# Kernel tuning notes

Measured on AMD Instinct MI355X. Metric: run time of the kernel, lower is better.

## Reference

```python
import jax, jax.numpy as jnp
import numpy as np
from jax import lax

TOP_K = 2
NHEAD = 8

def _ln(x, g, b, eps=1e-5):
    m = x.mean(-1, keepdims=True)
    v = x.var(-1, keepdims=True)
    return (x - m) / jnp.sqrt(v + eps) * g + b


def setup_inputs() -> dict:
    B, S, N = 32, 512, 32
    DT, D, E, HE, MO, LTX, LTCN, K = 64, 128, 16, 256, 128, 2, 4, 3
    keys = iter(jax.random.split(jax.random.key(0), 96))
    def rn(shape, s=0.05):
        return (jax.random.normal(next(keys), shape, jnp.float32) * s)
    inp = {}
    inp['x_features_globally_std'] = jax.random.normal(next(keys), (B, S, N), jnp.float32)
    counts = jax.random.randint(next(keys), (B,), 8, N + 1)
    inp['sensor_mask'] = (jnp.arange(N)[None, :] < counts[:, None]).astype(jnp.float32)
    inp['proj_w'] = rn((1, DT)); inp['proj_b'] = jnp.zeros(DT)
    inp['tcn_w1'] = rn((LTCN, DT, DT, K)); inp['tcn_b1'] = jnp.zeros((LTCN, DT))
    inp['tcn_w2'] = rn((LTCN, DT, DT, K)); inp['tcn_b2'] = jnp.zeros((LTCN, DT))
    inp['tcn_ln_g'] = jnp.ones(DT); inp['tcn_ln_b'] = jnp.zeros(DT)
    inp['pool_w'] = rn((DT, D)); inp['pool_b'] = jnp.zeros(D)
    inp['pos_inter'] = rn((1, N, D), 0.02)
    inp['tx_ln1_g'] = jnp.ones((LTX, D)); inp['tx_ln1_b'] = jnp.zeros((LTX, D))
    inp['tx_qkv_w'] = rn((LTX, D, 3 * D)); inp['tx_qkv_b'] = jnp.zeros((LTX, 3 * D))
    inp['tx_out_w'] = rn((LTX, D, D)); inp['tx_out_b'] = jnp.zeros((LTX, D))
    inp['tx_ln2_g'] = jnp.ones((LTX, D)); inp['tx_ln2_b'] = jnp.zeros((LTX, D))
    inp['tx_ff1_w'] = rn((LTX, D, 2 * D)); inp['tx_ff1_b'] = jnp.zeros((LTX, 2 * D))
    inp['tx_ff2_w'] = rn((LTX, 2 * D, D)); inp['tx_ff2_b'] = jnp.zeros((LTX, D))
    inp['tx_fln_g'] = jnp.ones(D); inp['tx_fln_b'] = jnp.zeros(D)
    inp['exp_w1'] = rn((E, D, HE)); inp['exp_b1'] = jnp.zeros((E, HE))
    inp['exp_w2'] = rn((E, HE, MO)); inp['exp_b2'] = jnp.zeros((E, MO))
    inp['gate_f_w'] = rn((2 * D, E)); inp['gate_f_b'] = jnp.zeros(E)
    inp['gate_fail_w'] = rn((2 * D, E)); inp['gate_fail_b'] = jnp.zeros(E)
    inp['gate_rca_w'] = rn((D, E)); inp['gate_rca_b'] = jnp.zeros(E)
    inp['pred_w'] = rn((DT + D + MO, 3)); inp['pred_b'] = jnp.zeros(3)
    inp['fail_w'] = rn((MO, 3)); inp['fail_b'] = jnp.zeros(3)
    inp['rca_w'] = rn((DT + D + MO, 1)); inp['rca_b'] = jnp.zeros(1)
    return inp


def reference(x_features_globally_std, sensor_mask, proj_w, proj_b, tcn_w1, tcn_b1, tcn_w2, tcn_b2,
              tcn_ln_g, tcn_ln_b, pool_w, pool_b, pos_inter, tx_ln1_g, tx_ln1_b, tx_qkv_w, tx_qkv_b,
              tx_out_w, tx_out_b, tx_ln2_g, tx_ln2_b, tx_ff1_w, tx_ff1_b, tx_ff2_w, tx_ff2_b,
              tx_fln_g, tx_fln_b, exp_w1, exp_b1, exp_w2, exp_b2, gate_f_w, gate_f_b,
              gate_fail_w, gate_fail_b, gate_rca_w, gate_rca_b, pred_w, pred_b, fail_w, fail_b, rca_w, rca_b):
    x = x_features_globally_std
    B, S, N = x.shape
    DT = proj_w.shape[1]; D = pool_w.shape[1]; E = gate_f_b.shape[0]
    K = tcn_w1.shape[-1]
    # per-sensor encoder: [B,S,N] -> [B*N, S, 1]
    x_enc = x.transpose(0, 2, 1).reshape(B * N, S, 1)
    h = x_enc @ proj_w + proj_b  # [BN,S,DT]
    # sinusoidal positional encoding
    pos = jnp.arange(S, dtype=jnp.float32)[:, None]
    div = jnp.exp(jnp.arange(0, DT, 2, dtype=jnp.float32) * (-np.log(10000.0) / DT))
    pe = jnp.zeros((S, DT), jnp.float32).at[:, 0::2].set(jnp.sin(pos * div)).at[:, 1::2].set(jnp.cos(pos * div))
    h = h + pe
    h = h.transpose(0, 2, 1)  # [BN, DT, S]
    for i in range(tcn_w1.shape[0]):
        dil = 2 ** i
        pad = (K - 1) * dil  # causal left pad == torch pad-both + trim right
        def conv(z, w, b):
            return lax.conv_general_dilated(z, w, (1,), [(pad, 0)], rhs_dilation=(dil,),
                                            dimension_numbers=('NCH', 'OIH', 'NCH')) + b[None, :, None]
        o = jax.nn.relu(conv(h, tcn_w1[i], tcn_b1[i]))
        o = jax.nn.relu(conv(o, tcn_w2[i], tcn_b2[i]))
        h = jax.nn.relu(o + h)  # proj_dim == tcn_out_dim -> no downsample
    h = _ln(h.transpose(0, 2, 1), tcn_ln_g, tcn_ln_b)  # [BN,S,DT]
    st = h.reshape(B, N, S, DT) * sensor_mask[:, :, None, None]
    pooled = st.mean(2)  # [B,N,DT]
    z = pooled @ pool_w + pool_b  # [B,N,D]
    z = z + pos_inter[0, :N]
    pad_mask = sensor_mask == 0  # [B,N] True = padded key
    hd = D // NHEAD
    for l in range(tx_qkv_w.shape[0]):
        y = _ln(z, tx_ln1_g[l], tx_ln1_b[l])
        qkv = y @ tx_qkv_w[l] + tx_qkv_b[l]
        q, k_, v = jnp.split(qkv, 3, -1)
        q = q.reshape(B, N, NHEAD, hd).transpose(0, 2, 1, 3)
        k_ = k_.reshape(B, N, NHEAD, hd).transpose(0, 2, 1, 3)
        v = v.reshape(B, N, NHEAD, hd).transpose(0, 2, 1, 3)
        scores = jnp.einsum('bhqd,bhkd->bhqk', q, k_) / jnp.sqrt(jnp.float32(hd))
        scores = jnp.where(pad_mask[:, None, None, :], -1e9, scores)
        attn = jax.nn.softmax(scores, -1)
        o = jnp.einsum('bhqk,bhkd->bhqd', attn, v).transpose(0, 2, 1, 3).reshape(B, N, D)
        z = z + o @ tx_out_w[l] + tx_out_b[l]
        y = _ln(z, tx_ln2_g[l], tx_ln2_b[l])
        z = z + jax.nn.relu(y @ tx_ff1_w[l] + tx_ff1_b[l]) @ tx_ff2_w[l] + tx_ff2_b[l]
    z = _ln(z, tx_fln_g, tx_fln_b)
    ctx = z * sensor_mask[..., None]  # [B,N,D]
    cnt = jnp.clip(sensor_mask.sum(1, keepdims=True), 1.0, None)
    mean_ctx = ctx.sum(1) / cnt
    var_ctx = (ctx ** 2).sum(1) / cnt - mean_ctx ** 2
    router_in = jnp.concatenate([mean_ctx, jnp.sqrt(jnp.clip(var_ctx, 1e-6, None))], -1)  # [B,2D]

    def moe(xin, gin, gw, gb):
        logits = gin @ gw + gb  # [n,E]
        tv, ti = lax.top_k(logits, TOP_K)
        w = jax.nn.softmax(tv, -1)
        h1 = jax.nn.relu(jnp.einsum('nd,edh->neh', xin, exp_w1) + exp_b1)
        allo = jnp.einsum('neh,eho->neo', h1, exp_w2) + exp_b2  # dense all-expert, per torch code
        sel = jnp.take_along_axis(allo, ti[:, :, None], 1)
        y = (sel * w[:, :, None]).sum(1)
        probs = jax.nn.softmax(logits, -1)
        frac = jnp.zeros((E,), probs.dtype).at[ti.reshape(-1)].add(1.0) / (xin.shape[0] * TOP_K)
        loss = E * (probs.mean(0) * frac).sum()
        return y, loss

    moe_f, aux_f = moe(mean_ctx, router_in, gate_f_w, gate_f_b)
    moe_fail, _ = moe(mean_ctx, router_in, gate_fail_w, gate_fail_b)
    tok = ctx.reshape(B * N, D)
    moe_rca, _ = moe(tok, tok, gate_rca_w, gate_rca_b)
    moe_rca = (moe_rca * sensor_mask.reshape(-1, 1)).reshape(B, N, -1)  # zero invalid tokens
    st_last = st[:, :, -1, :]  # [B,N,DT]
    moe_f_exp = jnp.broadcast_to(moe_f[:, None, :], (B, N, moe_f.shape[-1]))
    pred_in = jnp.concatenate([st_last, ctx, moe_f_exp], -1)
    pred = pred_in @ pred_w + pred_b  # [B,N,pred_horizons]
    fail = moe_fail @ fail_w + fail_b  # [B,fail_horizons]
    rca_in = jnp.concatenate([st_last, ctx, moe_rca], -1)
    rca = (rca_in @ rca_w + rca_b)[..., 0]  # [B,N]
    return pred, fail, rca, aux_f
```

## Files before the change

### kernel.cpp

```cpp
#include <hip/hip_runtime.h>
#include <hip/hip_bf16.h>
#include <math.h>

typedef short short8v __attribute__((ext_vector_type(8)));
typedef float f32x4 __attribute__((ext_vector_type(4)));
typedef unsigned short ushort4v __attribute__((ext_vector_type(4)));

__device__ inline float waveReduceSum(float v){
  #pragma unroll
  for (int off = 32; off > 0; off >>= 1) v += __shfl_xor(v, off, 64);
  return v;
}

__device__ inline unsigned short f2bf(float x){
  unsigned int u = __builtin_bit_cast(unsigned int, x);
  unsigned int r = (u + 0x7FFFu + ((u >> 16) & 1u)) >> 16;
  return (unsigned short)r;
}
__device__ inline float bf2f(unsigned short u){
  unsigned int w = ((unsigned int)u) << 16;
  return __builtin_bit_cast(float, w);
}

__global__ void init_kernel(const float* __restrict__ w1, const float* __restrict__ w2,
                            unsigned short* __restrict__ wf, float* __restrict__ petab){
  int idx = blockIdx.x * 256 + threadIdx.x;
  if (idx < 98304){
    int conv = idx / 12288;
    int r = idx % 12288;
    int tap = r >> 12;
    int kk  = (r >> 11) & 1;
    int ct  = (r >> 9) & 3;
    int lane= (r >> 3) & 63;
    int j   = r & 7;
    int layer = conv >> 1;
    const float* src = (conv & 1) ? w2 : w1;
    int co = (ct << 4) + (lane & 15);
    int ci = (kk << 5) + ((lane >> 4) << 3) + j;
    float v = src[((layer * 64 + co) * 64 + ci) * 3 + tap];
    unsigned short hi = f2bf(v);
    unsigned short lo = f2bf(v - bf2f(hi));
    size_t base = (size_t)conv * 24576 + (size_t)(((tap * 2 + kk) * 4 + ct) * 2) * 512 + lane * 8 + j;
    wf[base] = hi;
    wf[base + 512] = lo;
  } else if (idx < 131072){
    int p = idx - 98304;
    int t = p >> 6, c = p & 63;
    float ang = (float)t * expf(-0.14391156831f * (float)(c & ~1));
    petab[p] = (c & 1) ? cosf(ang) : sinf(ang);
  }
}

__global__ __launch_bounds__(512, 2) void tcn_persist_kernel(
    const float* __restrict__ x, const unsigned short* __restrict__ wfrag,
    const float* __restrict__ b1g, const float* __restrict__ b2g,
    const float* __restrict__ petab,
    const float* __restrict__ pw, const float* __restrict__ pb,
    const float* __restrict__ lng, const float* __restrict__ lnb,
    const float* __restrict__ maskg,
    float* __restrict__ pooled, float* __restrict__ stlast){
  constexpr int O_OFF = 139264;
  constexpr int P_OFF = 159744;
  __shared__ __align__(16) char lds[161792];
  const int tid = threadIdx.x;
  const int lane = tid & 63, wid = tid >> 6;
  const int cp = wid & 1, tsub = wid >> 1;
  const int bn = blockIdx.x;
  const int bb = bn >> 5, nn = bn & 31;

  for (int i = 0; i < 9; ++i){
    int idx = tid + i * 512;
    if (idx < 4352){
      int row = idx >> 3, cg = idx & 7;
      int t = row - 32;
      short8v vh = {0,0,0,0,0,0,0,0}, vl = {0,0,0,0,0,0,0,0};
      if (t >= 0){
        float xv = x[((size_t)bb << 14) + (t << 5) + nn];
        const float* per = petab + t * 64 + cg * 8;
        #pragma unroll
        for (int j = 0; j < 8; ++j){
          int c = cg * 8 + j;
          float val = fmaf(xv, pw[c], pb[c]) + per[j];
          unsigned short h = f2bf(val);
          vh[j] = (short)h;
          vl[j] = (short)f2bf(val - bf2f(h));
        }
      }
      int sw = (row & 7) << 4;
      int base = (row << 8) + (cg << 4);
      *(short8v*)(lds + (base ^ sw)) = vh;
      *(short8v*)(lds + ((base + 128) ^ sw)) = vl;
    }
  }

  const int cobase0 = ((2 * cp) << 4) + ((lane >> 4) << 2);
  const int cobase1 = ((2 * cp + 1) << 4) + ((lane >> 4) << 2);

  for (int layer = 0; layer < 4; ++layer){
    const int dil = 1 << layer;
    const int convbase = layer * 2;
    f32x4 b1v0 = *(const f32x4*)(b1g + (layer << 6) + cobase0);
    f32x4 b1v1 = *(const f32x4*)(b1g + (layer << 6) + cobase1);
    f32x4 b2v0 = *(const f32x4*)(b2g + (layer << 6) + cobase0);
    f32x4 b2v1 = *(const f32x4*)(b2g + (layer << 6) + cobase1);

    for (int ch = 7; ch >= 0; --ch){
      const int t0 = ch << 6;
      __syncthreads();

      short8v A1[3][2][2][2];
      #pragma unroll
      for (int tap = 0; tap < 3; ++tap)
        #pragma unroll
        for (int kk = 0; kk < 2; ++kk)
          #pragma unroll
          for (int cc = 0; cc < 2; ++cc)
            #pragma unroll
            for (int pl = 0; pl < 2; ++pl){
              int ct = 2 * cp + cc;
              A1[tap][kk][cc][pl] = *(const short8v*)(wfrag + (size_t)convbase * 24576 +
                  (size_t)((((tap * 2 + kk) * 4 + ct) * 2 + pl)) * 512 + lane * 8);
            }

      for (int S = 0; S < 2; ++S){
        int rbase = (S << 6) + (tsub << 4);
        if (rbase >= 80) continue;
        f32x4 acc0 = {0.f,0.f,0.f,0.f}, acc1 = {0.f,0.f,0.f,0.f};
        int orow = rbase + (lane & 15);
        int t_o = t0 - 16 + orow;
        #pragma unroll
        for (int tap = 0; tap < 3; ++tap){
          int hr = t_o - (2 - tap) * dil + 32;
          int sw = (hr & 7) << 4;
          #pragma unroll
          for (int kk = 0; kk < 2; ++kk){
            int base = (hr << 8) + (kk << 6) + ((lane >> 4) << 4);
            short8v Bhi = *(const short8v*)(lds + (base ^ sw));
            short8v Blo = *(const short8v*)(lds + ((base + 128) ^ sw));
            acc0 = __builtin_amdgcn_mfma_f32_16x16x32_bf16(A1[tap][kk][0][0], Bhi, acc0, 0, 0, 0);
            acc0 = __builtin_amdgcn_mfma_f32_16x16x32_bf16(A1[tap][kk][0][0], Blo, acc0, 0, 0, 0);
            acc0 = __builtin_amdgcn_mfma_f32_16x16x32_bf16(A1[tap][kk][0][1], Bhi, acc0, 0, 0, 0);
            acc1 = __builtin_amdgcn_mfma_f32_16x16x32_bf16(A1[tap][kk][1][0], Bhi, acc1, 0, 0, 0);
            acc1 = __builtin_amdgcn_mfma_f32_16x16x32_bf16(A1[tap][kk][1][0], Blo, acc1, 0, 0, 0);
            acc1 = __builtin_amdgcn_mfma_f32_16x16x32_bf16(A1[tap][kk][1][1], Bhi, acc1, 0, 0, 0);
          }
        }
        int swO = (orow & 7) << 4;
        #pragma unroll
        for (int cc = 0; cc < 2; ++cc){
          int cobase = (cc == 0) ? cobase0 : cobase1;
          ushort4v hi4, lo4;
          #pragma unroll
          for (int r = 0; r < 4; ++r){
            float a = (cc == 0) ? acc0[r] : acc1[r];
            float bv = (cc == 0) ? b1v0[r] : b1v1[r];
            float v = fmaxf(a + bv, 0.f);
            if (t_o < 0) v = 0.f;
            unsigned short h = f2bf(v);
            hi4[r] = h;
            lo4[r] = f2bf(v - bf2f(h));
          }
          int ob = O_OFF + (orow << 8) + (cobase << 1);
          *(ushort4v*)(lds + (ob ^ swO)) = hi4;
          *(ushort4v*)(lds + ((ob + 128) ^ swO)) = lo4;
        }
      }

      short8v A2[3][2][2][2];
      #pragma unroll
      for (int tap = 0; tap < 3; ++tap)
        #pragma unroll
        for (int kk = 0; kk < 2; ++kk)
          #pragma unroll
          for (int cc = 0; cc < 2; ++cc)
            #pragma unroll
            for (int pl = 0; pl < 2; ++pl){
              int ct = 2 * cp + cc;
              A2[tap][kk][cc][pl] = *(const short8v*)(wfrag + (size_t)(convbase + 1) * 24576 +
                  (size_t)((((tap * 2 + kk) * 4 + ct) * 2 + pl)) * 512 + lane * 8);
            }
      __syncthreads();

      {
        f32x4 acc0 = {0.f,0.f,0.f,0.f}, acc1 = {0.f,0.f,0.f,0.f};
        int tt = (tsub << 4) + (lane & 15);
        #pragma unroll
        for (int tap = 0; tap < 3; ++tap){
          int ol = tt + 16 - (2 - tap) * dil;
          int sw = (ol & 7) << 4;
          #pragma unroll
          for (int kk = 0; kk < 2; ++kk){
            int base = O_OFF + (ol << 8) + (kk << 6) + ((lane >> 4) << 4);
            short8v Bhi = *(const short8v*)(lds + (base ^ sw));
            short8v Blo = *(const short8v*)(lds + ((base + 128) ^ sw));
            acc0 = __builtin_amdgcn_mfma_f32_16x16x32_bf16(A2[tap][kk][0][0], Bhi, acc0, 0, 0, 0);
            acc0 = __builtin_amdgcn_mfma_f32_16x16x32_bf16(A2[tap][kk][0][0], Blo, acc0, 0, 0, 0);
            acc0 = __builtin_amdgcn_mfma_f32_16x16x32_bf16(A2[tap][kk][0][1], Bhi, acc0, 0, 0, 0);
            acc1 = __builtin_amdgcn_mfma_f32_16x16x32_bf16(A2[tap][kk][1][0], Bhi, acc1, 0, 0, 0);
            acc1 = __builtin_amdgcn_mfma_f32_16x16x32_bf16(A2[tap][kk][1][0], Blo, acc1, 0, 0, 0);
            acc1 = __builtin_amdgcn_mfma_f32_16x16x32_bf16(A2[tap][kk][1][1], Bhi, acc1, 0, 0, 0);
          }
        }
        int hr = t0 + tt + 32;
        int swH = (hr & 7) << 4;
        #pragma unroll
        for (int cc = 0; cc < 2; ++cc){
          int cobase = (cc == 0) ? cobase0 : cobase1;
          int rb = (hr << 8) + (cobase << 1);
          ushort4v rhi = *(const ushort4v*)(lds + (rb ^ swH));
          ushort4v rlo = *(const ushort4v*)(lds + ((rb + 128) ^ swH));
          ushort4v hi4, lo4;
          #pragma unroll
          for (int r = 0; r < 4; ++r){
            float a = (cc == 0) ? acc0[r] : acc1[r];
            float bv = (cc == 0) ? b2v0[r] : b2v1[r];
            float v = fmaxf(a + bv, 0.f);
            v = fmaxf(v + bf2f(rhi[r]) + bf2f(rlo[r]), 0.f);
            unsigned short h = f2bf(v);
            hi4[r] = h;
            lo4[r] = f2bf(v - bf2f(h));
          }
          *(ushort4v*)(lds + (rb ^ swH)) = hi4;
          *(ushort4v*)(lds + ((rb + 128) ^ swH)) = lo4;
        }
      }
    }
  }

  __syncthreads();
  {
    int s8 = tid >> 6, c = tid & 63;
    float gc = lng[c], bc = lnb[c];
    float mk = maskg[bn];
    float acc = 0.f, last = 0.f;
    for (int r0 = 0; r0 < 64; ++r0){
      int row = (s8 << 6) + r0;
      int hr = row + 32;
      int sw = (hr & 7) << 4;
      int base = (hr << 8) + (c << 1);
      float hi = bf2f(*(const unsigned short*)(lds + (base ^ sw)));
      float lo = bf2f(*(const unsigned short*)(lds + ((base + 128) ^ sw)));
      float val = hi + lo;
      float sum = val, sq = val * val;
      #pragma unroll
      for (int off = 32; off > 0; off >>= 1){
        sum += __shfl_xor(sum, off, 64);
        sq  += __shfl_xor(sq, off, 64);
      }
      float mean = sum * (1.f / 64.f);
      float var = sq * (1.f / 64.f) - mean * mean;
      float rstd = rsqrtf(var + 1e-5f);
      float o = (val - mean) * rstd * gc + bc;
      acc += o;
      if (row == 511) last = o;
    }
    *(float*)(lds + P_OFF + ((s8 << 6) + c) * 4) = acc;
    if (s8 == 7) stlast[(size_t)bn * 64 + c] = last * mk;
    __syncthreads();
    if (tid < 64){
      float tot = 0.f;
      #pragma unroll
      for (int ss = 0; ss < 8; ++ss) tot += *(const float*)(lds + P_OFF + ((ss << 6) + tid) * 4);
      pooled[(size_t)bn * 64 + tid] = tot * (1.f / 512.f) * mk;
    }
  }
}

__global__ __launch_bounds__(1024) void batch_kernel(
    const float* __restrict__ pooled, const float* __restrict__ maskg,
    const float* __restrict__ pool_w, const float* __restrict__ pool_b,
    const float* __restrict__ pos,
    const float* __restrict__ ln1g, const float* __restrict__ ln1b,
    const float* __restrict__ qkvw, const float* __restrict__ qkvb_g,
    const float* __restrict__ outw, const float* __restrict__ outb,
    const float* __restrict__ ln2g, const float* __restrict__ ln2b,
    const float* __restrict__ ff1w, const float* __restrict__ ff1b,
    const float* __restrict__ ff2w, const float* __restrict__ ff2b,
    const float* __restrict__ flng, const float* __restrict__ flnb,
    const float* __restrict__ ew1, const float* __restrict__ eb1,
    const float* __restrict__ ew2, const float* __restrict__ eb2,
    const float* __restrict__ gfw, const float* __restrict__ gfb,
    const float* __restrict__ gfailw, const float* __restrict__ gfailb,
    const float* __restrict__ failw, const float* __restrict__ failb,
    float* __restrict__ ctxg, float* __restrict__ moefg,
    float* __restrict__ logitsfg, int* __restrict__ tifg,
    float* __restrict__ outg){
  __shared__ float zf[32][128];
  __shared__ float ybuf[32][128];
  __shared__ float qkvb[32][385];
  __shared__ float sc[8][33][33];
  __shared__ float ps[32][64];
  __shared__ float msk[32];
  __shared__ float rin[256];
  __shared__ float meanc[128];
  __shared__ float h1all[4][256];
  __shared__ float oall[4][128];
  __shared__ float lf[16], lfail[16];
  __shared__ int   tisel[4];
  __shared__ float twsel[4];
  __shared__ float moefail[128];
  __shared__ float cntS;

  const int b = blockIdx.x;
  const int tid = threadIdx.x;
  const int lane = tid & 63;

  if (tid < 32) msk[tid] = maskg[b * 32 + tid];
  #pragma unroll
  for (int i = 0; i < 2; ++i){
    int item = tid + 1024 * i;
    int n = item >> 6, c = item & 63;
    ps[n][c] = pooled[(size_t)(b * 32 + n) * 64 + c];
  }
  __syncthreads();

  {
    int jb = tid & 63, nb = tid >> 6;
    float acc[2][2];
    #pragma unroll
    for (int nn = 0; nn < 2; ++nn)
      #pragma unroll
      for (int jj = 0; jj < 2; ++jj){
        int d = jb * 2 + jj, n = nb * 2 + nn;
        acc[nn][jj] = pool_b[d] + pos[n * 128 + d];
      }
    #pragma unroll 8
    for (int k = 0; k < 64; ++k){
      float w0 = pool_w[k * 128 + jb * 2], w1 = pool_w[k * 128 + jb * 2 + 1];
      #pragma unroll
      for (int nn = 0; nn < 2; ++nn){
        float y = ps[nb * 2 + nn][k];
        acc[nn][0] += y * w0; acc[nn][1] += y * w1;
      }
    }
    #pragma unroll
    for (int nn = 0; nn < 2; ++nn){
      zf[nb * 2 + nn][jb * 2]     = acc[nn][0];
      zf[nb * 2 + nn][jb * 2 + 1] = acc[nn][1];
    }
  }
  __syncthreads();

  for (int l = 0; l < 2; ++l){
    const float* Wq = qkvw + (size_t)l * 49152;
    const float* bq = qkvb_g + l * 384;
    const float* Wo = outw + (size_t)l * 16384;
    const float* bo = outb + l * 128;
    const float* W1 = ff1w + (size_t)l * 32768;
    const float* bf1 = ff1b + l * 256;
    const float* W2 = ff2w + (size_t)l * 32768;
    const float* bf2 = ff2b + l * 128;
    const float* g1 = ln1g + l * 128; const float* bb1 = ln1b + l * 128;
    const float* g2 = ln2g + l * 128; const float* bb2 = ln2b + l * 128;

    #pragma unroll
    for (int rr = 0; rr < 2; ++rr){
      int row = (tid >> 6) * 2 + rr;
      float x0 = zf[row][lane], x1 = zf[row][lane + 64];
      float mean = waveReduceSum(x0 + x1) * (1.f / 128.f);
      float d0 = x0 - mean, d1 = x1 - mean;
      float var = waveReduceSum(d0 * d0 + d1 * d1) * (1.f / 128.f);
      float rstd = rsqrtf(var + 1e-5f);
      ybuf[row][lane]      = d0 * rstd * g1[lane] + bb1[lane];
      ybuf[row][lane + 64] = d1 * rstd * g1[lane + 64] + bb1[lane + 64];
    }
    __syncthreads();

    {
      int jb = tid & 127, nb = tid >> 7;
      float acc[4][3];
      #pragma unroll
      for (int nn = 0; nn < 4; ++nn)
        #pragma unroll
        for (int jj = 0; jj < 3; ++jj) acc[nn][jj] = 0.f;
      #pragma unroll 8
      for (int k = 0; k < 128; ++k){
        float w0 = Wq[k * 384 + jb * 3], w1 = Wq[k * 384 + jb * 3 + 1], w2v = Wq[k * 384 + jb * 3 + 2];
        #pragma unroll
        for (int nn = 0; nn < 4; ++nn){
          float y = ybuf[nb * 4 + nn][k];
          acc[nn][0] += y * w0; acc[nn][1] += y * w1; acc[nn][2] += y * w2v;
        }
      }
      #pragma unroll
      for (int nn = 0; nn < 4; ++nn)
        #pragma unroll
        for (int jj = 0; jj < 3; ++jj)
          qkvb[nb * 4 + nn][jb * 3 + jj] = acc[nn][jj] + bq[jb * 3 + jj];
    }
    __syncthreads();

    #pragma unroll
    for (int i = 0; i < 8; ++i){
      int item = tid + 1024 * i;
      int hh = item >> 10, qi = (item >> 5) & 31, ki = item & 31;
      float a = 0.f;
      #pragma unroll
      for (int d = 0; d < 16; ++d) a += qkvb[qi][hh * 16 + d] * qkvb[ki][128 + hh * 16 + d];
      a *= 0.25f;
      if (msk[ki] == 0.f) a = -1e9f;
      sc[hh][qi][ki] = a;
    }
    __syncthreads();
    {
      int row = tid >> 2, q4 = tid & 3;
      int hh = row >> 5, qi = row & 31;
      float v[8];
      float m = -1e30f;
      #pragma unroll
      for (int j = 0; j < 8; ++j){ v[j] = sc[hh][qi][q4 * 8 + j]; m = fmaxf(m, v[j]); }
      m = fmaxf(m, __shfl_xor(m, 1, 64));
      m = fmaxf(m, __shfl_xor(m, 2, 64));
      float s = 0.f;
      #pragma unroll
      for (int j = 0; j < 8; ++j){ v[j] = expf(v[j] - m); s += v[j]; }
      s += __shfl_xor(s, 1, 64);
      s += __shfl_xor(s, 2, 64);
      float inv = 1.f / s;
      #pragma unroll
      for (int j = 0; j < 8; ++j) sc[hh][qi][q4 * 8 + j] = v[j] * inv;
    }
    __syncthreads();
    #pragma unroll
    for (int i = 0; i < 4; ++i){
      int item = tid + 1024 * i;
      int n = item >> 7, dd = item & 127, hh = dd >> 4;
      float o = 0.f;
      #pragma unroll
      for (int ki = 0; ki < 32; ++ki) o += sc[hh][n][ki] * qkvb[ki][256 + dd];
      ybuf[n][dd] = o;
    }
    __syncthreads();

    {
      int jb = tid & 63, nb = tid >> 6;
      float acc[2][2];
      #pragma unroll
      for (int nn = 0; nn < 2; ++nn){ acc[nn][0] = 0.f; acc[nn][1] = 0.f; }
      #pragma unroll 8
      for (int k = 0; k < 128; ++k){
        float w0 = Wo[k * 128 + jb * 2], w1 = Wo[k * 128 + jb * 2 + 1];
        #pragma unroll
        for (int nn = 0; nn < 2; ++nn){
          float y = ybuf[nb * 2 + nn][k];
          acc[nn][0] += y * w0; acc[nn][1] += y * w1;
        }
      }
      #pragma unroll
      for (int nn = 0; nn < 2; ++nn){
        zf[nb * 2 + nn][jb * 2]     += acc[nn][0] + bo[jb * 2];
        zf[nb * 2 + nn][jb * 2 + 1] += acc[nn][1] + bo[jb * 2 + 1];
      }
    }
    __syncthreads();

    #pragma unroll
    for (int rr = 0; rr < 2; ++rr){
      int row = (tid >> 6) * 2 + rr;
      float x0 = zf[row][lane], x1 = zf[row][lane + 64];
      float mean = waveReduceSum(x0 + x1) * (1.f / 128.f);
      float d0 = x0 - mean, d1 = x1 - mean;
      float var = waveReduceSum(d0 * d0 + d1 * d1) * (1.f / 128.f);
      float rstd = rsqrtf(var + 1e-5f);
      ybuf[row][lane]      = d0 * rstd * g2[lane] + bb2[lane];
      ybuf[row][lane + 64] = d1 * rstd * g2[lane + 64] + bb2[lane + 64];
    }
    __syncthreads();

    {
      int jb = tid & 127, nb = tid >> 7;
      float acc[4][2];
      #pragma unroll
      for (int nn = 0; nn < 4; ++nn){ acc[nn][0] = 0.f; acc[nn][1] = 0.f; }
      #pragma unroll 8
      for (int k = 0; k < 128; ++k){
        float w0 = W1[k * 256 + jb * 2], w1 = W1[k * 256 + jb * 2 + 1];
        #pragma unroll
        for (int nn = 0; nn < 4; ++nn){
          float y = ybuf[nb * 4 + nn][k];
          acc[nn][0] += y * w0; acc[nn][1] += y * w1;
        }
      }
      #pragma unroll
      for (int nn = 0; nn < 4; ++nn){
        qkvb[nb * 4 + nn][jb * 2]     = fmaxf(acc[nn][0] + bf1[jb * 2], 0.f);
        qkvb[nb * 4 + nn][jb * 2 + 1] = fmaxf(acc[nn][1] + bf1[jb * 2 + 1], 0.f);
      }
    }
    __syncthreads();

    {
      int jb = tid & 63, nb = tid >> 6;
      float acc[2][2];
      #pragma unroll
      for (int nn = 0; nn < 2; ++nn){ acc[nn][0] = 0.f; acc[nn][1] = 0.f; }
      #pragma unroll 8
      for (int k = 0; k < 256; ++k){
        float w0 = W2[k * 128 + jb * 2], w1 = W2[k * 128 + jb * 2 + 1];
        #pragma unroll
        for (int nn = 0; nn < 2; ++nn){
          float y = qkvb[nb * 2 + nn][k];
          acc[nn][0] += y * w0; acc[nn][1] += y * w1;
        }
      }
      #pragma unroll
      for (int nn = 0; nn < 2; ++nn){
        zf[nb * 2 + nn][jb * 2]     += acc[nn][0] + bf2[jb * 2];
        zf[nb * 2 + nn][jb * 2 + 1] += acc[nn][1] + bf2[jb * 2 + 1];
      }
    }
    __syncthreads();
  }

  #pragma unroll
  for (int rr = 0; rr < 2; ++rr){
    int row = (tid >> 6) * 2 + rr;
    float x0 = zf[row][lane], x1 = zf[row][lane + 64];
    float mean = waveReduceSum(x0 + x1) * (1.f / 128.f);
    float d0 = x0 - mean, d1 = x1 - mean;
    float var = waveReduceSum(d0 * d0 + d1 * d1) * (1.f / 128.f);
    float rstd = rsqrtf(var + 1e-5f);
    float mk = msk[row];
    ybuf[row][lane]      = (d0 * rstd * flng[lane] + flnb[lane]) * mk;
    ybuf[row][lane + 64] = (d1 * rstd * flng[lane + 64] + flnb[lane + 64]) * mk;
  }
  if (tid == 0){
    float c = 0.f;
    for (int n = 0; n < 32; ++n) c += maskg[b * 32 + n];
    cntS = fmaxf(c, 1.f);
  }
  __syncthreads();
  #pragma unroll
  for (int i = 0; i < 4; ++i){
    int item = tid + 1024 * i;
    int n = item >> 7, d = item & 127;
    ctxg[(size_t)(b * 32 + n) * 128 + d] = ybuf[n][d];
  }
  if (tid < 128){
    float s = 0.f, s2 = 0.f;
    #pragma unroll 8
    for (int n = 0; n < 32; ++n){ float v = ybuf[n][tid]; s += v; s2 += v * v; }
    float mean = s / cntS;
    float var = s2 / cntS - mean * mean;
    meanc[tid] = mean;
    rin[tid] = mean;
    rin[128 + tid] = sqrtf(fmaxf(var, 1e-6f));
  }
  __syncthreads();
  {
    int g = tid >> 9;
    int e = (tid >> 5) & 15, kk = tid & 31;
    const float* gw = g ? gfailw : gfw;
    float a = 0.f;
    #pragma unroll
    for (int j = 0; j < 8; ++j){
      int k = kk * 8 + j;
      a += rin[k] * gw[k * 16 + e];
    }
    a += __shfl_xor(a, 1, 64);  a += __shfl_xor(a, 2, 64);
    a += __shfl_xor(a, 4, 64);  a += __shfl_xor(a, 8, 64);
    a += __shfl_xor(a, 16, 64);
    if (kk == 0){
      if (g == 0){
        float r = a + gfb[e];
        lf[e] = r;
        logitsfg[b * 16 + e] = r;
      } else {
        lfail[e] = a + gfailb[e];
      }
    }
  }
  __syncthreads();
  if (tid < 2){
    const float* lg = (tid == 0) ? lf : lfail;
    int i0 = 0; float v0 = lg[0];
    for (int e = 1; e < 16; ++e) if (lg[e] > v0){ v0 = lg[e]; i0 = e; }
    int i1 = -1; float v1 = -1e30f;
    for (int e = 0; e < 16; ++e) if (e != i0 && lg[e] > v1){ v1 = lg[e]; i1 = e; }
    float e1 = expf(v1 - v0);
    float den = 1.f / (1.f + e1);
    tisel[tid * 2] = i0; tisel[tid * 2 + 1] = i1;
    twsel[tid * 2] = den; twsel[tid * 2 + 1] = e1 * den;
    if (tid == 0){ tifg[b * 2] = i0; tifg[b * 2 + 1] = i1; }
  }
  __syncthreads();
  {
    int sel = tid >> 8, h = tid & 255;
    int e = tisel[sel];
    float a = eb1[e * 256 + h];
    #pragma unroll 8
    for (int k = 0; k < 128; ++k) a += meanc[k] * ew1[(size_t)(e * 128 + k) * 256 + h];
    h1all[sel][h] = fmaxf(a, 0.f);
  }
  __syncthreads();
  if (tid < 512){
    int sel = tid >> 7, d = tid & 127;
    int e = tisel[sel];
    float o = eb2[e * 128 + d];
    #pragma unroll 8
    for (int k = 0; k < 256; ++k) o += h1all[sel][k] * ew2[(size_t)(e * 256 + k) * 128 + d];
    oall[sel][d] = twsel[sel] * o;
  }
  __syncthreads();
  if (tid < 128){
    moefg[b * 128 + tid] = oall[0][tid] + oall[1][tid];
    moefail[tid] = oall[2][tid] + oall[3][tid];
  }
  __syncthreads();
  if (tid < 3){
    float a = failb[tid];
    for (int k = 0; k < 128; ++k) a += moefail[k] * failw[k * 3 + tid];
    outg[3072 + b * 3 + tid] = a;
  }
}

__global__ void gate_kernel(const float* __restrict__ gin, const float* __restrict__ gw,
                            const float* __restrict__ gb, int ntok, int K,
                            int* __restrict__ ti, float* __restrict__ tw,
                            float* __restrict__ logits_out){
  int tok = blockIdx.x * 64 + threadIdx.x;
  if (tok >= ntok) return;
  float acc[16];
  #pragma unroll
  for (int e = 0; e < 16; ++e) acc[e] = gb[e];
  const float* gr = gin + (size_t)tok * K;
  #pragma unroll 4
  for (int k = 0; k < K; ++k){
    float gv = gr[k];
    #pragma unroll
    for (int e = 0; e < 16; ++e) acc[e] = fmaf(gv, gw[k*16 + e], acc[e]);
  }
  if (logits_out){
    #pragma unroll
    for (int e = 0; e < 16; ++e) logits_out[tok*16 + e] = acc[e];
  }
  int i0 = 0; float v0 = acc[0];
  #pragma unroll
  for (int e = 1; e < 16; ++e) if (acc[e] > v0){ v0 = acc[e]; i0 = e; }
  int i1 = -1; float v1 = -1e30f;
  #pragma unroll
  for (int e = 0; e < 16; ++e) if (e != i0 && acc[e] > v1){ v1 = acc[e]; i1 = e; }
  float e1 = expf(v1 - v0);
  float den = 1.f / (1.f + e1);
  ti[tok*2] = i0; ti[tok*2+1] = i1;
  tw[tok*2] = den; tw[tok*2+1] = e1 * den;
}

__global__ void moe_expert_kernel(const float* __restrict__ xin, const int* __restrict__ ti,
                                  const float* __restrict__ tw,
                                  const float* __restrict__ w1, const float* __restrict__ b1,
                                  const float* __restrict__ w2, const float* __restrict__ b2,
                                  const float* __restrict__ mask, float* __restrict__ yout){
  int tok = blockIdx.x;
  int tid = threadIdx.x;
  __shared__ float xs[128];
  __shared__ float h1[256];
  if (tid < 128) xs[tid] = xin[(size_t)tok*128 + tid];
  __syncthreads();
  float accv = 0.f;
  for (int kkk = 0; kkk < 2; ++kkk){
    int e = ti[tok*2 + kkk];
    float wv = tw[tok*2 + kkk];
    float a = b1[e*256 + tid];
    #pragma unroll 8
    for (int k = 0; k < 128; ++k) a = fmaf(xs[k], w1[(size_t)(e*128 + k)*256 + tid], a);
    __syncthreads();
    h1[tid] = fmaxf(a, 0.f);
    __syncthreads();
    if (tid < 128){
      float o = b2[e*128 + tid];
      #pragma unroll 8
      for (int k = 0; k < 256; ++k) o = fmaf(h1[k], w2[(size_t)(e*256 + k)*128 + tid], o);
      accv += wv * o;
    }
  }
  if (tid < 128){
    if (mask) accv *= mask[tok];
    yout[(size_t)tok*128 + tid] = accv;
  }
}

__global__ void aux_kernel(const float* __restrict__ logits, const int* __restrict__ ti,
                           float* __restrict__ out_scalar){
  if (threadIdx.x != 0 || blockIdx.x != 0) return;
  float pm[16];
  for (int e = 0; e < 16; ++e) pm[e] = 0.f;
  for (int i = 0; i < 32; ++i){
    const float* row = logits + i*16;
    float m = -1e30f;
    for (int e = 0; e < 16; ++e) m = fmaxf(m, row[e]);
    float s = 0.f;
    float ex[16];
    for (int e = 0; e < 16; ++e){ ex[e] = expf(row[e] - m); s += ex[e]; }
    for (int e = 0; e < 16; ++e) pm[e] += ex[e] / s;
  }
  float cnt[16];
  for (int e = 0; e < 16; ++e) cnt[e] = 0.f;
  for (int i = 0; i < 64; ++i) cnt[ti[i]] += 1.f;
  float loss = 0.f;
  for (int e = 0; e < 16; ++e) loss += (pm[e] / 32.f) * (cnt[e] / 64.f);
  out_scalar[0] = 16.f * loss;
}

__global__ void heads_kernel(const float* __restrict__ st_last, const float* __restrict__ ctx,
                             const float* __restrict__ moe_f, const float* __restrict__ moe_rca,
                             const float* __restrict__ pred_w, const float* __restrict__ pred_b,
                             const float* __restrict__ rca_w, const float* __restrict__ rca_b,
                             float* __restrict__ out){
  int bn = blockIdx.x * 256 + threadIdx.x;
  if (bn >= 1024) return;
  int b = bn >> 5;
  float p0 = pred_b[0], p1 = pred_b[1], p2 = pred_b[2];
  float r = rca_b[0];
  #pragma unroll 4
  for (int i = 0; i < 64; ++i){
    float v = st_last[(size_t)bn*64 + i];
    p0 = fmaf(v, pred_w[i*3+0], p0); p1 = fmaf(v, pred_w[i*3+1], p1); p2 = fmaf(v, pred_w[i*3+2], p2);
    r = fmaf(v, rca_w[i], r);
  }
  #pragma unroll 4
  for (int i = 0; i < 128; ++i){
    float v = ctx[(size_t)bn*128 + i];
    int ii = 64 + i;
    p0 = fmaf(v, pred_w[ii*3+0], p0); p1 = fmaf(v, pred_w[ii*3+1], p1); p2 = fmaf(v, pred_w[ii*3+2], p2);
    r = fmaf(v, rca_w[ii], r);
  }
  #pragma unroll 4
  for (int i = 0; i < 128; ++i){
    int ii = 192 + i;
    float vp = moe_f[(size_t)b*128 + i];
    p0 = fmaf(vp, pred_w[ii*3+0], p0); p1 = fmaf(vp, pred_w[ii*3+1], p1); p2 = fmaf(vp, pred_w[ii*3+2], p2);
    float vr = moe_rca[(size_t)bn*128 + i];
    r = fmaf(vr, rca_w[ii], r);
  }
  out[bn*3+0] = p0; out[bn*3+1] = p1; out[bn*3+2] = p2;
  out[3168 + bn] = r;
}

extern "C" void kernel_launch(void* const* d_in, const int* in_sizes, int n_in,
                              void* d_out, int out_size, void* d_ws, size_t ws_size,
                              hipStream_t stream){
  const float* x        = (const float*)d_in[0];
  const float* mask     = (const float*)d_in[1];
  const float* proj_w   = (const float*)d_in[2];
  const float* proj_b   = (const float*)d_in[3];
  const float* tcn_w1   = (const float*)d_in[4];
  const float* tcn_b1   = (const float*)d_in[5];
  const float* tcn_w2   = (const float*)d_in[6];
  const float* tcn_b2   = (const float*)d_in[7];
  const float* tcn_ln_g = (const float*)d_in[8];
  const float* tcn_ln_b = (const float*)d_in[9];
  const float* pool_w   = (const float*)d_in[10];
  const float* pool_b   = (const float*)d_in[11];
  const float* pos_inter= (const float*)d_in[12];
  const float* tx_ln1_g = (const float*)d_in[13];
  const float* tx_ln1_b = (const float*)d_in[14];
  const float* tx_qkv_w = (const float*)d_in[15];
  const float* tx_qkv_b = (const float*)d_in[16];
  const float* tx_out_w = (const float*)d_in[17];
  const float* tx_out_b = (const float*)d_in[18];
  const float* tx_ln2_g = (const float*)d_in[19];
  const float* tx_ln2_b = (const float*)d_in[20];
  const float* tx_ff1_w = (const float*)d_in[21];
  const float* tx_ff1_b = (const float*)d_in[22];
  const float* tx_ff2_w = (const float*)d_in[23];
  const float* tx_ff2_b = (const float*)d_in[24];
  const float* tx_fln_g = (const float*)d_in[25];
  const float* tx_fln_b = (const float*)d_in[26];
  const float* exp_w1   = (const float*)d_in[27];
  const float* exp_b1   = (const float*)d_in[28];
  const float* exp_w2   = (const float*)d_in[29];
  const float* exp_b2   = (const float*)d_in[30];
  const float* gate_f_w = (const float*)d_in[31];
  const float* gate_f_b = (const float*)d_in[32];
  const float* gate_fail_w = (const float*)d_in[33];
  const float* gate_fail_b = (const float*)d_in[34];
  const float* gate_rca_w  = (const float*)d_in[35];
  const float* gate_rca_b  = (const float*)d_in[36];
  const float* pred_w   = (const float*)d_in[37];
  const float* pred_b   = (const float*)d_in[38];
  const float* fail_w   = (const float*)d_in[39];
  const float* fail_b   = (const float*)d_in[40];
  const float* rca_w    = (const float*)d_in[41];
  const float* rca_b    = (const float*)d_in[42];
  float* out = (float*)d_out;
  float* W = (float*)d_ws;

  const size_t o_pooled  = 0;
  const size_t o_stlast  = 65536;
  const size_t o_ctx     = 131072;
  const size_t o_moef    = 262144;
  const size_t o_moerca  = 266240;
  const size_t o_logitsf = 397312;
  const size_t o_tif     = 397824;
  const size_t o_twrca   = 397888;
  const size_t o_tirca   = 399936;
  const size_t o_petab   = 401984;
  unsigned short* wfragU = (unsigned short*)(W + 434752);

  init_kernel<<<512, 256, 0, stream>>>(tcn_w1, tcn_w2, wfragU, W + o_petab);

  tcn_persist_kernel<<<1024, 512, 0, stream>>>(
      x, wfragU, tcn_b1, tcn_b2, W + o_petab, proj_w, proj_b,
      tcn_ln_g, tcn_ln_b, mask, W + o_pooled, W + o_stlast);

  batch_kernel<<<32, 1024, 0, stream>>>(
      W + o_pooled, mask, pool_w, pool_b, pos_inter,
      tx_ln1_g, tx_ln1_b, tx_qkv_w, tx_qkv_b, tx_out_w, tx_out_b,
      tx_ln2_g, tx_ln2_b, tx_ff1_w, tx_ff1_b, tx_ff2_w, tx_ff2_b,
      tx_fln_g, tx_fln_b,
      exp_w1, exp_b1, exp_w2, exp_b2,
      gate_f_w, gate_f_b, gate_fail_w, gate_fail_b, fail_w, fail_b,
      W + o_ctx, W + o_moef, W + o_logitsf, (int*)(W + o_tif), out);

  gate_kernel<<<16, 64, 0, stream>>>(W + o_ctx, gate_rca_w, gate_rca_b, 1024, 128,
                                     (int*)(W + o_tirca), W + o_twrca, nullptr);
  moe_expert_kernel<<<1024, 256, 0, stream>>>(W + o_ctx, (int*)(W + o_tirca), W + o_twrca,
                                              exp_w1, exp_b1, exp_w2, exp_b2, mask, W + o_moerca);

  aux_kernel<<<1, 64, 0, stream>>>(W + o_logitsf, (int*)(W + o_tif), out + 4192);
  heads_kernel<<<4, 256, 0, stream>>>(W + o_stlast, W + o_ctx, W + o_moef, W + o_moerca,
                                      pred_w, pred_b, rca_w, rca_b, out);
}
```

Baseline: 944.1 us.

## Double TCN block to 1024 threads with one output tile per wave

The TCN kernel now launches 1024 threads per block, so each wave handles one 16-channel output tile instead of two. This halves per-wave weight fragments and accumulators, and layers become templated for compile-time dilation. The pooled-reduction scratch reuses the intermediate buffer region, which adds a barrier, and the LayerNorm pass is split across 16 waves. Each wave has less MFMA work to hide latency, and register pressure under the 1024-thread launch bound may cause spills.

```diff
diff --git a/kernel.cpp b/kernel.cpp
--- a/kernel.cpp
+++ b/kernel.cpp
@@ -21,6 +21,8 @@
   unsigned int w = ((unsigned int)u) << 16;
   return __builtin_bit_cast(float, w);
 }
+
+#define TCN_O_OFF 139264
 
 __global__ void init_kernel(const float* __restrict__ w1, const float* __restrict__ w2,
                             unsigned short* __restrict__ wf, float* __restrict__ petab){
@@ -51,7 +53,117 @@
   }
 }
 
-__global__ __launch_bounds__(512, 2) void tcn_persist_kernel(
+template<int LAYER>
+__device__ __forceinline__ void run_layer(
+    char* lds, const unsigned short* __restrict__ wfrag,
+    const float* __restrict__ b1g, const float* __restrict__ b2g,
+    int lane, int coq, int tsub){
+  constexpr int DIL = 1 << LAYER;
+  constexpr int CONVBASE = LAYER * 2;
+  const int cobase = (coq << 4) + ((lane >> 4) << 2);
+  const f32x4 b1v = *(const f32x4*)(b1g + (LAYER << 6) + cobase);
+  const f32x4 b2v = *(const f32x4*)(b2g + (LAYER << 6) + cobase);
+
+  for (int ch = 7; ch >= 0; --ch){
+    const int t0 = ch << 6;
+    __syncthreads();
+
+    short8v A1[3][2][2];
+    #pragma unroll
+    for (int tap = 0; tap < 3; ++tap)
+      #pragma unroll
+      for (int kk = 0; kk < 2; ++kk)
+        #pragma unroll
+        for (int pl = 0; pl < 2; ++pl)
+          A1[tap][kk][pl] = *(const short8v*)(wfrag + (size_t)CONVBASE * 24576 +
+              (size_t)((((tap * 2 + kk) * 4 + coq) * 2 + pl)) * 512 + lane * 8);
+
+    #pragma unroll
+    for (int S = 0; S < 2; ++S){
+      int rbase = (S << 6) + (tsub << 4);
+      if (rbase < 80){
+        f32x4 acc = {0.f,0.f,0.f,0.f};
+        int orow = rbase + (lane & 15);
+        int t_o = t0 - 16 + orow;
+        #pragma unroll
+        for (int tap = 0; tap < 3; ++tap){
+          int hr = t_o - (2 - tap) * DIL + 32;
+          int sw = (hr & 7) << 4;
+          #pragma unroll
+          for (int kk = 0; kk < 2; ++kk){
+            int base = (hr << 8) + (kk << 6) + ((lane >> 4) << 4);
+            short8v Bhi = *(const short8v*)(lds + (base ^ sw));
+            short8v Blo = *(const short8v*)(lds + ((base + 128) ^ sw));
+            acc = __builtin_amdgcn_mfma_f32_16x16x32_bf16(A1[tap][kk][0], Bhi, acc, 0, 0, 0);
+            acc = __builtin_amdgcn_mfma_f32_16x16x32_bf16(A1[tap][kk][0], Blo, acc, 0, 0, 0);
+            acc = __builtin_amdgcn_mfma_f32_16x16x32_bf16(A1[tap][kk][1], Bhi, acc, 0, 0, 0);
+          }
+        }
+        int swO = (orow & 7) << 4;
+        ushort4v hi4, lo4;
+        #pragma unroll
+        for (int r = 0; r < 4; ++r){
+          float v = fmaxf(acc[r] + b1v[r], 0.f);
+          if (t_o < 0) v = 0.f;
+          unsigned short h = f2bf(v);
+          hi4[r] = h;
+          lo4[r] = f2bf(v - bf2f(h));
+        }
+        int ob = TCN_O_OFF + (orow << 8) + (cobase << 1);
+        *(ushort4v*)(lds + (ob ^ swO)) = hi4;
+        *(ushort4v*)(lds + ((ob + 128) ^ swO)) = lo4;
+      }
+    }
+
+    short8v A2[3][2][2];
+    #pragma unroll
+    for (int tap = 0; tap < 3; ++tap)
+      #pragma unroll
+      for (int kk = 0; kk < 2; ++kk)
+        #pragma unroll
+        for (int pl = 0; pl < 2; ++pl)
+          A2[tap][kk][pl] = *(const short8v*)(wfrag + (size_t)(CONVBASE + 1) * 24576 +
+              (size_t)((((tap * 2 + kk) * 4 + coq) * 2 + pl)) * 512 + lane * 8);
+    __syncthreads();
+
+    {
+      f32x4 acc = {0.f,0.f,0.f,0.f};
+      int tt = (tsub << 4) + (lane & 15);
+      #pragma unroll
+      for (int tap = 0; tap < 3; ++tap){
+        int ol = tt + 16 - (2 - tap) * DIL;
+        int sw = (ol & 7) << 4;
+        #pragma unroll
+        for (int kk = 0; kk < 2; ++kk){
+          int base = TCN_O_OFF + (ol << 8) + (kk << 6) + ((lane >> 4) << 4);
+          short8v Bhi = *(const short8v*)(lds + (base ^ sw));
+          short8v Blo = *(const short8v*)(lds + ((base + 128) ^ sw));
+          acc = __builtin_amdgcn_mfma_f32_16x16x32_bf16(A2[tap][kk][0], Bhi, acc, 0, 0, 0);
+          acc = __builtin_amdgcn_mfma_f32_16x16x32_bf16(A2[tap][kk][0], Blo, acc, 0, 0, 0);
+          acc = __builtin_amdgcn_mfma_f32_16x16x32_bf16(A2[tap][kk][1], Bhi, acc, 0, 0, 0);
+        }
+      }
+      int hr = t0 + tt + 32;
+      int swH = (hr & 7) << 4;
+      int rb = (hr << 8) + (cobase << 1);
+      ushort4v rhi = *(const ushort4v*)(lds + (rb ^ swH));
+      ushort4v rlo = *(const ushort4v*)(lds + ((rb + 128) ^ swH));
+      ushort4v hi4, lo4;
+      #pragma unroll
+      for (int r = 0; r < 4; ++r){
+        float v = fmaxf(acc[r] + b2v[r], 0.f);
+        v = fmaxf(v + bf2f(rhi[r]) + bf2f(rlo[r]), 0.f);
+        unsigned short h = f2bf(v);
+        hi4[r] = h;
+        lo4[r] = f2bf(v - bf2f(h));
+      }
+      *(ushort4v*)(lds + (rb ^ swH)) = hi4;
+      *(ushort4v*)(lds + ((rb + 128) ^ swH)) = lo4;
+    }
+  }
+}
+
+__global__ __launch_bounds__(1024, 4) void tcn_persist_kernel(
     const float* __restrict__ x, const unsigned short* __restrict__ wfrag,
     const float* __restrict__ b1g, const float* __restrict__ b2g,
     const float* __restrict__ petab,
@@ -59,17 +171,16 @@
     const float* __restrict__ lng, const float* __restrict__ lnb,
     const float* __restrict__ maskg,
     float* __restrict__ pooled, float* __restrict__ stlast){
-  constexpr int O_OFF = 139264;
-  constexpr int P_OFF = 159744;
-  __shared__ __align__(16) char lds[161792];
+  __shared__ __align__(16) char lds[159744];
   const int tid = threadIdx.x;
   const int lane = tid & 63, wid = tid >> 6;
-  const int cp = wid & 1, tsub = wid >> 1;
+  const int coq = wid & 3, tsub = wid >> 2;
   const int bn = blockIdx.x;
   const int bb = bn >> 5, nn = bn & 31;
 
-  for (int i = 0; i < 9; ++i){
-    int idx = tid + i * 512;
+  #pragma unroll
+  for (int i = 0; i < 5; ++i){
+    int idx = tid + i * 1024;
     if (idx < 4352){
       int row = idx >> 3, cg = idx & 7;
       int t = row - 32;
@@ -93,148 +204,19 @@
     }
   }
 
-  const int cobase0 = ((2 * cp) << 4) + ((lane >> 4) << 2);
-  const int cobase1 = ((2 * cp + 1) << 4) + ((lane >> 4) << 2);
-
-  for (int layer = 0; layer < 4; ++layer){
-    const int dil = 1 << layer;
-    const int convbase = layer * 2;
-    f32x4 b1v0 = *(const f32x4*)(b1g + (layer << 6) + cobase0);
-    f32x4 b1v1 = *(const f32x4*)(b1g + (layer << 6) + cobase1);
-    f32x4 b2v0 = *(const f32x4*)(b2g + (layer << 6) + cobase0);
-    f32x4 b2v1 = *(const f32x4*)(b2g + (layer << 6) + cobase1);
-
-    for (int ch = 7; ch >= 0; --ch){
-      const int t0 = ch << 6;
-      __syncthreads();
-
-      short8v A1[3][2][2][2];
-      #pragma unroll
-      for (int tap = 0; tap < 3; ++tap)
-        #pragma unroll
-        for (int kk = 0; kk < 2; ++kk)
-          #pragma unroll
-          for (int cc = 0; cc < 2; ++cc)
-            #pragma unroll
-            for (int pl = 0; pl < 2; ++pl){
-              int ct = 2 * cp + cc;
-              A1[tap][kk][cc][pl] = *(const short8v*)(wfrag + (size_t)convbase * 24576 +
-                  (size_t)((((tap * 2 + kk) * 4 + ct) * 2 + pl)) * 512 + lane * 8);
-            }
-
-      for (int S = 0; S < 2; ++S){
-        int rbase = (S << 6) + (tsub << 4);
-        if (rbase >= 80) continue;
-        f32x4 acc0 = {0.f,0.f,0.f,0.f}, acc1 = {0.f,0.f,0.f,0.f};
-        int orow = rbase + (lane & 15);
-        int t_o = t0 - 16 + orow;
-        #pragma unroll
-        for (int tap = 0; tap < 3; ++tap){
-          int hr = t_o - (2 - tap) * dil + 32;
-          int sw = (hr & 7) << 4;
-          #pragma unroll
-          for (int kk = 0; kk < 2; ++kk){
-            int base = (hr << 8) + (kk << 6) + ((lane >> 4) << 4);
-            short8v Bhi = *(const short8v*)(lds + (base ^ sw));
-            short8v Blo = *(const short8v*)(lds + ((base + 128) ^ sw));
-            acc0 = __builtin_amdgcn_mfma_f32_16x16x32_bf16(A1[tap][kk][0][0], Bhi, acc0, 0, 0, 0);
-            acc0 = __builtin_amdgcn_mfma_f32_16x16x32_bf16(A1[tap][kk][0][0], Blo, acc0, 0, 0, 0);
-            acc0 = __builtin_amdgcn_mfma_f32_16x16x32_bf16(A1[tap][kk][0][1], Bhi, acc0, 0, 0, 0);
-            acc1 = __builtin_amdgcn_mfma_f32_16x16x32_bf16(A1[tap][kk][1][0], Bhi, acc1, 0, 0, 0);
-            acc1 = __builtin_amdgcn_mfma_f32_16x16x32_bf16(A1[tap][kk][1][0], Blo, acc1, 0, 0, 0);
-            acc1 = __builtin_amdgcn_mfma_f32_16x16x32_bf16(A1[tap][kk][1][1], Bhi, acc1, 0, 0, 0);
-          }
-        }
-        int swO = (orow & 7) << 4;
-        #pragma unroll
-        for (int cc = 0; cc < 2; ++cc){
-          int cobase = (cc == 0) ? cobase0 : cobase1;
-          ushort4v hi4, lo4;
-          #pragma unroll
-          for (int r = 0; r < 4; ++r){
-            float a = (cc == 0) ? acc0[r] : acc1[r];
-            float bv = (cc == 0) ? b1v0[r] : b1v1[r];
-            float v = fmaxf(a + bv, 0.f);
-            if (t_o < 0) v = 0.f;
-            unsigned short h = f2bf(v);
-            hi4[r] = h;
-            lo4[r] = f2bf(v - bf2f(h));
-          }
-          int ob = O_OFF + (orow << 8) + (cobase << 1);
-          *(ushort4v*)(lds + (ob ^ swO)) = hi4;
-          *(ushort4v*)(lds + ((ob + 128) ^ swO)) = lo4;
-        }
-      }
-
-      short8v A2[3][2][2][2];
-      #pragma unroll
-      for (int tap = 0; tap < 3; ++tap)
-        #pragma unroll
-        for (int kk = 0; kk < 2; ++kk)
-          #pragma unroll
-          for (int cc = 0; cc < 2; ++cc)
-            #pragma unroll
-            for (int pl = 0; pl < 2; ++pl){
-              int ct = 2 * cp + cc;
-              A2[tap][kk][cc][pl] = *(const short8v*)(wfrag + (size_t)(convbase + 1) * 24576 +
-                  (size_t)((((tap * 2 + kk) * 4 + ct) * 2 + pl)) * 512 + lane * 8);
-            }
-      __syncthreads();
-
-      {
-        f32x4 acc0 = {0.f,0.f,0.f,0.f}, acc1 = {0.f,0.f,0.f,0.f};
-        int tt = (tsub << 4) + (lane & 15);
-        #pragma unroll
-        for (int tap = 0; tap < 3; ++tap){
-          int ol = tt + 16 - (2 - tap) * dil;
-          int sw = (ol & 7) << 4;
-          #pragma unroll
-          for (int kk = 0; kk < 2; ++kk){
-            int base = O_OFF + (ol << 8) + (kk << 6) + ((lane >> 4) << 4);
-            short8v Bhi = *(const short8v*)(lds + (base ^ sw));
-            short8v Blo = *(const short8v*)(lds + ((base + 128) ^ sw));
-            acc0 = __builtin_amdgcn_mfma_f32_16x16x32_bf16(A2[tap][kk][0][0], Bhi, acc0, 0, 0, 0);
-            acc0 = __builtin_amdgcn_mfma_f32_16x16x32_bf16(A2[tap][kk][0][0], Blo, acc0, 0, 0, 0);
-            acc0 = __builtin_amdgcn_mfma_f32_16x16x32_bf16(A2[tap][kk][0][1], Bhi, acc0, 0, 0, 0);
-            acc1 = __builtin_amdgcn_mfma_f32_16x16x32_bf16(A2[tap][kk][1][0], Bhi, acc1, 0, 0, 0);
-            acc1 = __builtin_amdgcn_mfma_f32_16x16x32_bf16(A2[tap][kk][1][0], Blo, acc1, 0, 0, 0);
-            acc1 = __builtin_amdgcn_mfma_f32_16x16x32_bf16(A2[tap][kk][1][1], Bhi, acc1, 0, 0, 0);
-          }
-        }
-        int hr = t0 + tt + 32;
-        int swH = (hr & 7) << 4;
-        #pragma unroll
-        for (int cc = 0; cc < 2; ++cc){
-          int cobase = (cc == 0) ? cobase0 : cobase1;
-          int rb = (hr << 8) + (cobase << 1);
-          ushort4v rhi = *(const ushort4v*)(lds + (rb ^ swH));
-          ushort4v rlo = *(const ushort4v*)(lds + ((rb + 128) ^ swH));
-          ushort4v hi4, lo4;
-          #pragma unroll
-          for (int r = 0; r < 4; ++r){
-            float a = (cc == 0) ? acc0[r] : acc1[r];
-            float bv = (cc == 0) ? b2v0[r] : b2v1[r];
-            float v = fmaxf(a + bv, 0.f);
-            v = fmaxf(v + bf2f(rhi[r]) + bf2f(rlo[r]), 0.f);
-            unsigned short h = f2bf(v);
-            hi4[r] = h;
-            lo4[r] = f2bf(v - bf2f(h));
-          }
-          *(ushort4v*)(lds + (rb ^ swH)) = hi4;
-          *(ushort4v*)(lds + ((rb + 128) ^ swH)) = lo4;
-        }
-      }
-    }
-  }
+  run_layer<0>(lds, wfrag, b1g, b2g, lane, coq, tsub);
+  run_layer<1>(lds, wfrag, b1g, b2g, lane, coq, tsub);
+  run_layer<2>(lds, wfrag, b1g, b2g, lane, coq, tsub);
+  run_layer<3>(lds, wfrag, b1g, b2g, lane, coq, tsub);
 
   __syncthreads();
   {
     int s8 = tid >> 6, c = tid & 63;
     float gc = lng[c], bc = lnb[c];
     float mk = maskg[bn];
-    float acc = 0.f, last = 0.f;
-    for (int r0 = 0; r0 < 64; ++r0){
-      int row = (s8 << 6) + r0;
+    float acc = 0.f;
+    for (int r0 = 0; r0 < 32; ++r0){
+      int row = (s8 << 5) + r0;
       int hr = row + 32;
       int sw = (hr & 7) << 4;
       int base = (hr << 8) + (c << 1);
@@ -252,15 +234,15 @@
       float rstd = rsqrtf(var + 1e-5f);
       float o = (val - mean) * rstd * gc + bc;
       acc += o;
-      if (row == 511) last = o;
-    }
-    *(float*)(lds + P_OFF + ((s8 << 6) + c) * 4) = acc;
-    if (s8 == 7) stlast[(size_t)bn * 64 + c] = last * mk;
+      if (row == 511) stlast[(size_t)bn * 64 + c] = o * mk;
+    }
+    __syncthreads();
+    *(float*)(lds + TCN_O_OFF + ((s8 << 6) + c) * 4) = acc;
     __syncthreads();
     if (tid < 64){
       float tot = 0.f;
       #pragma unroll
-      for (int ss = 0; ss < 8; ++ss) tot += *(const float*)(lds + P_OFF + ((ss << 6) + tid) * 4);
+      for (int ss = 0; ss < 16; ++ss) tot += *(const float*)(lds + TCN_O_OFF + ((ss << 6) + tid) * 4);
       pooled[(size_t)bn * 64 + tid] = tot * (1.f / 512.f) * mk;
     }
   }
@@ -800,7 +782,7 @@
 
   init_kernel<<<512, 256, 0, stream>>>(tcn_w1, tcn_w2, wfragU, W + o_petab);
 
-  tcn_persist_kernel<<<1024, 512, 0, stream>>>(
+  tcn_persist_kernel<<<1024, 1024, 0, stream>>>(
       x, wfragU, tcn_b1, tcn_b2, W + o_petab, proj_w, proj_b,
       tcn_ln_g, tcn_ln_b, mask, W + o_pooled, W + o_stlast);
 
```

New measurement: 1.106 ms. +17.1%, slower.
